# Kernel optimization log

Measured on AMD Instinct MI355X. Metric: run time of the kernel, lower is better.

Reference implementation:

```python
import jax, jax.numpy as jnp
import numpy as np

KERNEL_SIZES = [5, 5]   # kernel_sizes init arg
CIN, COUT = 8, 8        # in_channels / out_channels of each Kernel


def setup_inputs() -> dict:
    key = jax.random.key(0)
    ks = jax.random.split(key, 11)
    B, L, n_types, d = 4, 512, 100, 8
    h1, h2, h3, F = 16, 32, 16, 2
    times = jnp.sort(jax.random.uniform(ks[0], (B, L), dtype=jnp.float32), axis=1)
    features = jax.random.randint(ks[1], (B, L), 0, n_types)
    emb = jax.random.normal(ks[2], (n_types, d), dtype=jnp.float32) * 0.5
    W1 = jax.random.normal(ks[3], (F, 1, h1), dtype=jnp.float32) * 0.5
    B1 = jax.random.normal(ks[4], (F, h1), dtype=jnp.float32) * 0.1
    W2 = jax.random.normal(ks[5], (F, h1, h2), dtype=jnp.float32) * 0.3
    B2 = jax.random.normal(ks[6], (F, h2), dtype=jnp.float32) * 0.1
    W3 = jax.random.normal(ks[7], (F, h2, h3), dtype=jnp.float32) * 0.3
    B3 = jax.random.normal(ks[8], (F, h3), dtype=jnp.float32) * 0.1
    W4 = jax.random.normal(ks[9], (F, h3, CIN * COUT), dtype=jnp.float32) * 0.3
    B4 = jax.random.normal(ks[10], (F, CIN * COUT), dtype=jnp.float32) * 0.1
    return {"times": times, "features": features, "emb": emb,
            "W1": W1, "B1": B1, "W2": W2, "B2": B2,
            "W3": W3, "B3": B3, "W4": W4, "B4": B4}


def reference(times, features, emb, W1, B1, W2, B2, W3, B3, W4, B4):
    B, L = times.shape
    ii = jnp.arange(L)[:, None]
    jj = jnp.arange(L)[None, :]
    x = emb[features]  # (B, L, CIN)
    for f, k in enumerate(KERNEL_SIZES):
        # triu(ones, diagonal=-k): keep j >= i - k
        triu = (jj >= ii - k).astype(times.dtype)
        # band mask = tril(diag=-1) * triu(diag=-k): i-k <= j <= i-1
        band = ((jj <= ii - 1) & (jj >= ii - k)).astype(times.dtype)
        # S[b,i,j] = relu(t_i - t_j) * triu
        dt = jnp.maximum(times[:, :, None] - times[:, None, :], 0.0) * triu
        s = dt[..., None]                          # (B,L,L,1)
        h = jax.nn.relu(s @ W1[f] + B1[f])         # (B,L,L,h1)
        h = jax.nn.relu(h @ W2[f] + B2[f])         # (B,L,L,h2)
        h = jax.nn.relu(h @ W3[f] + B3[f])         # (B,L,L,h3)
        kv = (h @ W4[f] + B4[f]).reshape(B, L, L, CIN, COUT)
        kv = kv * band[None, :, :, None, None]
        # out[b,i,d] = sum_{j,c} x[b,i,c] * kv[b,i,j,c,d]
        x = jnp.einsum('bic,bijcd->bid', x, kv)
    return x
```

## Files before the change

### kernel.cpp

```cpp
#include <hip/hip_runtime.h>


#define KSZ 5

__global__ __launch_bounds__(64) void ccnn_h3_kernel(
    const float* __restrict__ times,
    const float* __restrict__ W1, const float* __restrict__ B1,
    const float* __restrict__ W2, const float* __restrict__ B2,
    const float* __restrict__ W3, const float* __restrict__ B3,
    float* __restrict__ H)
{
    __shared__ __align__(16) float sW1[16];
    __shared__ __align__(16) float sB1[16];
    __shared__ __align__(16) float sW2[512];
    __shared__ __align__(16) float sB2[32];
    __shared__ __align__(16) float sW3[512];
    __shared__ __align__(16) float sB3[16];

    const int tid = threadIdx.x;
    const int f   = (blockIdx.x >= 256) ? 1 : 0;

    for (int idx = tid; idx < 512; idx += 64) {
        sW2[idx] = W2[f * 512 + idx];
        sW3[idx] = W3[f * 512 + idx];
    }
    if (tid < 16) {
        sW1[tid] = W1[f * 16 + tid];
        sB1[tid] = B1[f * 16 + tid];
        sB3[tid] = B3[f * 16 + tid];
    }
    if (tid < 32) sB2[tid] = B2[f * 32 + tid];
    __syncthreads();

    const int gid = blockIdx.x * 64 + tid;
    const int rem = gid & 16383;
    const int bi  = rem >> 3;
    const int jo  = rem & 7;
    const int i   = bi & 511;
    const int b   = bi >> 9;
    const int j   = i - 1 - jo;
    const bool valid = (jo < KSZ) && (j >= 0);

    float s = 0.0f;
    if (valid) {
        float ti = times[b * 512 + i];
        float tj = times[b * 512 + j];
        s = fmaxf(ti - tj, 0.0f);
    }

    float h1[16];
    #pragma unroll
    for (int o = 0; o < 16; ++o)
        h1[o] = fmaxf(fmaf(s, sW1[o], sB1[o]), 0.0f);

    float h2[32];
    #pragma unroll
    for (int o4 = 0; o4 < 8; ++o4) {
        float4 a = *(const float4*)&sB2[o4 * 4];
        #pragma unroll
        for (int ii = 0; ii < 16; ++ii) {
            const float4 w = *(const float4*)&sW2[ii * 32 + o4 * 4];
            a.x = fmaf(h1[ii], w.x, a.x);
            a.y = fmaf(h1[ii], w.y, a.y);
            a.z = fmaf(h1[ii], w.z, a.z);
            a.w = fmaf(h1[ii], w.w, a.w);
        }
        h2[o4 * 4 + 0] = fmaxf(a.x, 0.0f);
        h2[o4 * 4 + 1] = fmaxf(a.y, 0.0f);
        h2[o4 * 4 + 2] = fmaxf(a.z, 0.0f);
        h2[o4 * 4 + 3] = fmaxf(a.w, 0.0f);
    }

    float h3[16];
    #pragma unroll
    for (int o4 = 0; o4 < 4; ++o4) {
        float4 a = *(const float4*)&sB3[o4 * 4];
        #pragma unroll
        for (int ii = 0; ii < 32; ++ii) {
            const float4 w = *(const float4*)&sW3[ii * 16 + o4 * 4];
            a.x = fmaf(h2[ii], w.x, a.x);
            a.y = fmaf(h2[ii], w.y, a.y);
            a.z = fmaf(h2[ii], w.z, a.z);
            a.w = fmaf(h2[ii], w.w, a.w);
        }
        h3[o4 * 4 + 0] = fmaxf(a.x, 0.0f);
        h3[o4 * 4 + 1] = fmaxf(a.y, 0.0f);
        h3[o4 * 4 + 2] = fmaxf(a.z, 0.0f);
        h3[o4 * 4 + 3] = fmaxf(a.w, 0.0f);
    }

    #pragma unroll
    for (int o = 0; o < 16; ++o)
        if (!valid) h3[o] = 0.0f;

    #pragma unroll
    for (int m = 1; m <= 4; m <<= 1) {
        #pragma unroll
        for (int o = 0; o < 16; ++o)
            h3[o] += __shfl_xor(h3[o], m, 64);
    }

    if (jo == 0) {
        float4* dst = (float4*)&H[(f * 2048 + bi) * 16];
        dst[0] = make_float4(h3[0],  h3[1],  h3[2],  h3[3]);
        dst[1] = make_float4(h3[4],  h3[5],  h3[6],  h3[7]);
        dst[2] = make_float4(h3[8],  h3[9],  h3[10], h3[11]);
        dst[3] = make_float4(h3[12], h3[13], h3[14], h3[15]);
    }
}

__global__ __launch_bounds__(256) void ccnn_out_kernel(
    const int*   __restrict__ features,
    const float* __restrict__ emb,
    const float* __restrict__ W4,
    const float* __restrict__ B4,
    const float* __restrict__ H,
    float* __restrict__ out)
{
    const int lane = threadIdx.x & 63;
    const int w    = threadIdx.x >> 6;
    const int bi   = blockIdx.x * 4 + w;
    const int i    = bi & 511;
    const int c    = lane >> 3;
    const float n  = (float)min(i, KSZ);

    const int feat = features[bi];
    float x = emb[feat * 8 + c];

    float xr = 0.0f;
    #pragma unroll
    for (int f = 0; f < 2; ++f) {
        const float* Hp = &H[(f * 2048 + bi) * 16];
        float m = n * B4[f * 64 + lane];
        #pragma unroll
        for (int ii = 0; ii < 16; ++ii)
            m = fmaf(Hp[ii], W4[f * 1024 + ii * 64 + lane], m);
        float p = x * m;
        p += __shfl_xor(p, 8, 64);
        p += __shfl_xor(p, 16, 64);
        p += __shfl_xor(p, 32, 64);
        xr = p;
        x = __shfl(xr, lane >> 3, 64);
    }

    if (lane < 8) out[bi * 8 + lane] = xr;
}

extern "C" void kernel_launch(void* const* d_in, const int* in_sizes, int n_in,
                              void* d_out, int out_size, void* d_ws, size_t ws_size,
                              hipStream_t stream) {
    const float* times    = (const float*)d_in[0];
    const int*   features = (const int*)  d_in[1];
    const float* emb      = (const float*)d_in[2];
    const float* W1       = (const float*)d_in[3];
    const float* B1       = (const float*)d_in[4];
    const float* W2       = (const float*)d_in[5];
    const float* B2       = (const float*)d_in[6];
    const float* W3       = (const float*)d_in[7];
    const float* B3       = (const float*)d_in[8];
    const float* W4       = (const float*)d_in[9];
    const float* B4       = (const float*)d_in[10];
    float* out = (float*)d_out;
    float* H   = (float*)d_ws;

    ccnn_h3_kernel<<<512, 64, 0, stream>>>(times, W1, B1, W2, B2, W3, B3, H);
    ccnn_out_kernel<<<512, 256, 0, stream>>>(features, emb, W4, B4, H, out);
}
```

Before: 89.79 us.

## Fuse MLP-hidden and output kernels into one launch via shared memory

Merges the two kernels into a single kernel in which each 128-thread block computes the h3 features for both filters (one wavefront per filter) for 8 rows. The block stores them in shared memory and then runs the W4 contraction and the sequential two-layer einsum from there. This removes the second kernel launch and the global-memory round trip through the H workspace. In exchange each block loads both filters' weights, including W4, into shared memory, only 256 blocks are launched, and the output stage runs serially over 4 rows per wavefront.

Result: no change. 89.37 us (-0.5%).

```diff
diff --git a/kernel.cpp b/kernel.cpp
--- a/kernel.cpp
+++ b/kernel.cpp
@@ -3,63 +3,69 @@
 
 #define KSZ 5
 
-__global__ __launch_bounds__(64) void ccnn_h3_kernel(
+__global__ __launch_bounds__(128) void ccnn_fused_kernel(
     const float* __restrict__ times,
+    const int*   __restrict__ features,
+    const float* __restrict__ emb,
     const float* __restrict__ W1, const float* __restrict__ B1,
     const float* __restrict__ W2, const float* __restrict__ B2,
     const float* __restrict__ W3, const float* __restrict__ B3,
-    float* __restrict__ H)
+    const float* __restrict__ W4, const float* __restrict__ B4,
+    float* __restrict__ out)
 {
-    __shared__ __align__(16) float sW1[16];
-    __shared__ __align__(16) float sB1[16];
-    __shared__ __align__(16) float sW2[512];
-    __shared__ __align__(16) float sB2[32];
-    __shared__ __align__(16) float sW3[512];
-    __shared__ __align__(16) float sB3[16];
+    __shared__ __align__(16) float sW1[2][16];
+    __shared__ __align__(16) float sB1[2][16];
+    __shared__ __align__(16) float sW2[2][512];
+    __shared__ __align__(16) float sB2[2][32];
+    __shared__ __align__(16) float sW3[2][512];
+    __shared__ __align__(16) float sB3[2][16];
+    __shared__ __align__(16) float sW4[2][1024];
+    __shared__ __align__(16) float sB4[2][64];
+    __shared__ __align__(16) float sH[2][8][16];
 
     const int tid = threadIdx.x;
-    const int f   = (blockIdx.x >= 256) ? 1 : 0;
 
-    for (int idx = tid; idx < 512; idx += 64) {
-        sW2[idx] = W2[f * 512 + idx];
-        sW3[idx] = W3[f * 512 + idx];
+    for (int idx = tid; idx < 1024; idx += 128) {
+        (&sW2[0][0])[idx] = W2[idx];
+        (&sW3[0][0])[idx] = W3[idx];
     }
-    if (tid < 16) {
-        sW1[tid] = W1[f * 16 + tid];
-        sB1[tid] = B1[f * 16 + tid];
-        sB3[tid] = B3[f * 16 + tid];
+    for (int idx = tid; idx < 2048; idx += 128)
+        (&sW4[0][0])[idx] = W4[idx];
+    if (tid < 32) {
+        (&sW1[0][0])[tid] = W1[tid];
+        (&sB1[0][0])[tid] = B1[tid];
+        (&sB3[0][0])[tid] = B3[tid];
     }
-    if (tid < 32) sB2[tid] = B2[f * 32 + tid];
+    if (tid < 64)  (&sB2[0][0])[tid] = B2[tid];
+    (&sB4[0][0])[tid & 127] = B4[tid & 127];
     __syncthreads();
 
-    const int gid = blockIdx.x * 64 + tid;
-    const int rem = gid & 16383;
-    const int bi  = rem >> 3;
-    const int jo  = rem & 7;
-    const int i   = bi & 511;
-    const int b   = bi >> 9;
-    const int j   = i - 1 - jo;
+    const int f    = tid >> 6;
+    const int lane = tid & 63;
+    const int bil  = lane >> 3;
+    const int jo   = lane & 7;
+    const int bi   = blockIdx.x * 8 + bil;
+    const int i    = bi & 511;
+    const int b    = bi >> 9;
+    const int j    = i - 1 - jo;
     const bool valid = (jo < KSZ) && (j >= 0);
 
     float s = 0.0f;
-    if (valid) {
-        float ti = times[b * 512 + i];
-        float tj = times[b * 512 + j];
-        s = fmaxf(ti - tj, 0.0f);
-    }
+    if (valid)
+        s = fmaxf(times[b * 512 + i] - times[b * 512 + j], 0.0f);
 
     float h1[16];
     #pragma unroll
     for (int o = 0; o < 16; ++o)
-        h1[o] = fmaxf(fmaf(s, sW1[o], sB1[o]), 0.0f);
+        h1[o] = fmaxf(fmaf(s, sW1[f][o], sB1[f][o]), 0.0f);
 
     float h2[32];
     #pragma unroll
     for (int o4 = 0; o4 < 8; ++o4) {
-        float4 a = *(const float4*)&sB2[o4 * 4];
+        float4 a = *(const float4*)&sB2[f][o4 * 4];
         #pragma unroll
         for (int ii = 0; ii < 16; ++ii) {
-            const float4 w = *(const float4*)&sW2[ii * 32 + o4 * 4];
+            const float4 w = *(const float4*)&sW2[f][ii * 32 + o4 * 4];
             a.x = fmaf(h1[ii], w.x, a.x);
             a.y = fmaf(h1[ii], w.y, a.y);
             a.z = fmaf(h1[ii], w.z, a.z);
@@ -74,10 +80,10 @@
     float h3[16];
     #pragma unroll
     for (int o4 = 0; o4 < 4; ++o4) {
-        float4 a = *(const float4*)&sB3[o4 * 4];
+        float4 a = *(const float4*)&sB3[f][o4 * 4];
         #pragma unroll
         for (int ii = 0; ii < 32; ++ii) {
-            const float4 w = *(const float4*)&sW3[ii * 16 + o4 * 4];
+            const float4 w = *(const float4*)&sW3[f][ii * 16 + o4 * 4];
             a.x = fmaf(h2[ii], w.x, a.x);
             a.y = fmaf(h2[ii], w.y, a.y);
             a.z = fmaf(h2[ii], w.z, a.z);
@@ -92,7 +98,6 @@
     #pragma unroll
     for (int o = 0; o < 16; ++o)
         if (!valid) h3[o] = 0.0f;
-
     #pragma unroll
     for (int m = 1; m <= 4; m <<= 1) {
         #pragma unroll
@@ -101,49 +106,40 @@
     }
 
     if (jo == 0) {
-        float4* dst = (float4*)&H[(f * 2048 + bi) * 16];
+        float4* dst = (float4*)&sH[f][bil][0];
         dst[0] = make_float4(h3[0],  h3[1],  h3[2],  h3[3]);
         dst[1] = make_float4(h3[4],  h3[5],  h3[6],  h3[7]);
         dst[2] = make_float4(h3[8],  h3[9],  h3[10], h3[11]);
         dst[3] = make_float4(h3[12], h3[13], h3[14], h3[15]);
     }
-}
+    __syncthreads();
 
-__global__ __launch_bounds__(256) void ccnn_out_kernel(
-    const int*   __restrict__ features,
-    const float* __restrict__ emb,
-    const float* __restrict__ W4,
-    const float* __restrict__ B4,
-    const float* __restrict__ H,
-    float* __restrict__ out)
-{
-    const int lane = threadIdx.x & 63;
-    const int w    = threadIdx.x >> 6;
-    const int bi   = blockIdx.x * 4 + w;
-    const int i    = bi & 511;
-    const int c    = lane >> 3;
-    const float n  = (float)min(i, KSZ);
+    const int c = lane >> 3;
+    #pragma unroll
+    for (int q = 0; q < 4; ++q) {
+        const int bil2 = f * 4 + q;
+        const int bi2  = blockIdx.x * 8 + bil2;
+        const int i2   = bi2 & 511;
+        const float n  = (float)min(i2, KSZ);
 
-    const int feat = features[bi];
-    float x = emb[feat * 8 + c];
-
-    float xr = 0.0f;
-    #pragma unroll
-    for (int f = 0; f < 2; ++f) {
-        const float* Hp = &H[(f * 2048 + bi) * 16];
-        float m = n * B4[f * 64 + lane];
+        const int feat = features[bi2];
+        float x  = emb[feat * 8 + c];
+        float xr = 0.0f;
         #pragma unroll
-        for (int ii = 0; ii < 16; ++ii)
-            m = fmaf(Hp[ii], W4[f * 1024 + ii * 64 + lane], m);
-        float p = x * m;
-        p += __shfl_xor(p, 8, 64);
-        p += __shfl_xor(p, 16, 64);
-        p += __shfl_xor(p, 32, 64);
-        xr = p;
-        x = __shfl(xr, lane >> 3, 64);
+        for (int ff = 0; ff < 2; ++ff) {
+            float m = n * sB4[ff][lane];
+            #pragma unroll
+            for (int ii = 0; ii < 16; ++ii)
+                m = fmaf(sH[ff][bil2][ii], sW4[ff][ii * 64 + lane], m);
+            float p = x * m;
+            p += __shfl_xor(p, 8, 64);
+            p += __shfl_xor(p, 16, 64);
+            p += __shfl_xor(p, 32, 64);
+            xr = p;
+            x  = __shfl(xr, lane >> 3, 64);
+        }
+        if (lane < 8) out[bi2 * 8 + lane] = xr;
     }
-
-    if (lane < 8) out[bi * 8 + lane] = xr;
 }
 
 extern "C" void kernel_launch(void* const* d_in, const int* in_sizes, int n_in,
@@ -161,8 +157,7 @@
     const float* W4       = (const float*)d_in[9];
     const float* B4       = (const float*)d_in[10];
     float* out = (float*)d_out;
-    float* H   = (float*)d_ws;
 
-    ccnn_h3_kernel<<<512, 64, 0, stream>>>(times, W1, B1, W2, B2, W3, B3, H);
-    ccnn_out_kernel<<<512, 256, 0, stream>>>(features, emb, W4, B4, H, out);
+    ccnn_fused_kernel<<<256, 128, 0, stream>>>(
+        times, features, emb, W1, B1, W2, B2, W3, B3, W4, B4, out);
 }
```
